# Optimization experiments

Measured on AMD Instinct MI355X. Metric: run time of the kernel, lower is better.

The kernel has to match this reference:

```python
import jax, jax.numpy as jnp
import numpy as np

EMB_DIM = 64
DICT_SIZE = 512
MOMENTUM = 0.99
EPS = 1e-05


def setup_inputs() -> dict:
    key = jax.random.key(0)
    k1, k2 = jax.random.split(key)
    inp = jax.random.normal(k1, (32, EMB_DIM, 64, 64), dtype=jnp.float32)
    embed = jax.random.normal(k2, (DICT_SIZE, EMB_DIM), dtype=jnp.float32)
    cluster_size = jnp.zeros((DICT_SIZE,), dtype=jnp.float32)
    embed_avg = embed.T  # torch: self.embed.T.clone()
    return {"input": inp, "embed": embed, "cluster_size": cluster_size, "embed_avg": embed_avg}


def reference(input, embed, cluster_size, embed_avg):
    b, c, h, w = input.shape
    D = embed.shape[0]
    # torch: input.transpose(1, -1).reshape(-1, emb_dim)  -> row order (b, w, h)
    flatten = jnp.swapaxes(input, 1, -1).reshape(-1, c)  # (N, c)
    # negative squared L2 scores (largest == nearest), as in _torch_knn
    scores = 2.0 * (flatten @ embed.T)                     # (N, D)
    scores = scores - jnp.sum(embed * embed, axis=1)[None, :]
    scores = scores - jnp.sum(flatten * flatten, axis=1)[:, None]
    ids_flat = jnp.argmax(scores, axis=1)                  # (N,) int
    # torch: ids.view(b, h, w) (quirk: flatten order is (b,w,h); h==w so shapes match)
    ids = ids_flat.reshape(b, h, w)
    # lookup: F.embedding(ids, embed).transpose(1, -1); the two transposes cancel
    quantized = jnp.swapaxes(embed[ids_flat].reshape(b, w, h, c), 1, -1)  # (b, c, h, w)
    commit_loss = jnp.mean(jnp.square(input - quantized))
    # EMA codebook statistics (training branch, done under no_grad in torch)
    onehot_sum = jax.ops.segment_sum(jnp.ones_like(ids_flat, dtype=flatten.dtype), ids_flat, num_segments=D)  # (D,)
    embed_sum = jax.ops.segment_sum(flatten, ids_flat, num_segments=D).T  # (c, D) == flatten.T @ onehot
    new_cluster_size = cluster_size * MOMENTUM + onehot_sum * (1.0 - MOMENTUM)
    new_embed_avg = embed_avg * MOMENTUM + embed_sum * (1.0 - MOMENTUM)
    n = jnp.sum(new_cluster_size)
    cs = n * (new_cluster_size + EPS) / (n + D * EPS)
    new_embed = new_embed_avg.T / cs[:, None]
    return quantized, commit_loss, ids, new_embed, new_cluster_size, new_embed_avg
```

## Files before the change

### kernel.cpp

```cpp
#include <hip/hip_runtime.h>

#define EMB 64
#define DICT 512
#define HW 4096
#define NPTS (32 * HW)
#define MOM 0.99f
#define OMOM 0.01f
#define EPSV 1e-5f

typedef float v4f __attribute__((ext_vector_type(4)));
typedef unsigned int uint;
typedef uint uint4v __attribute__((ext_vector_type(4)));
typedef short short8 __attribute__((ext_vector_type(8)));
typedef __bf16 bf16x8 __attribute__((ext_vector_type(8)));
typedef float f32x4 __attribute__((ext_vector_type(4)));

#define WS_COMMIT 0
#define WS_COUNTS 64
#define WS_ESUM   1024
#define WS_ZERO_FLOATS 33792
#define WS_EE     33792
#define WS_EHG    34320
#define WS_IDS    67600

#define PS 520
#define TB 4160

#define ESCALE 65536.0f
#define EINV   (1.0f / 65536.0f)

__device__ __forceinline__ uint bf16rne(float x) {
    uint u = __float_as_uint(x);
    return (u + 0x7fffu + ((u >> 16) & 1u)) >> 16;
}

__device__ __forceinline__ bf16x8 ldfragg(const uint* s, int idx) {
    return __builtin_bit_cast(bf16x8, *(const short8*)(s + idx));
}

__global__ __launch_bounds__(256) void vq_prep(const float* __restrict__ embed,
                                               float* __restrict__ ws,
                                               uint* __restrict__ ehg,
                                               float* __restrict__ ee) {
    int t = threadIdx.x;
    int blk = blockIdx.x;
    for (int i = blk * 256 + t; i < WS_ZERO_FLOATS; i += 32 * 256) ws[i] = 0.f;

    int jl = t >> 4;
    int ci = t & 15;
    int j  = blk * 16 + jl;
    float nrm = 0.f;
    #pragma unroll
    for (int it = 0; it < 2; ++it) {
        int c2 = ci + it * 16;
        float x0 = embed[j * 64 + 2 * c2];
        float x1 = embed[j * 64 + 2 * c2 + 1];
        nrm = fmaf(x0, x0, nrm);
        nrm = fmaf(x1, x1, nrm);
        uint h0 = bf16rne(x0), h1 = bf16rne(x1);
        int plane = (c2 >> 4) * 4 + ((c2 >> 2) & 3);
        int idx = (j >> 7) * TB + plane * PS + (j & 127) * 4 + (c2 & 3);
        ehg[idx] = h0 | (h1 << 16);
    }
    #pragma unroll
    for (int off = 8; off > 0; off >>= 1) nrm += __shfl_xor(nrm, off, 16);
    if (ci == 0) ee[j] = nrm;
}

__global__ __launch_bounds__(256, 4) void vq_argmax(
    const float* __restrict__ input, const uint* __restrict__ ehg,
    const float* __restrict__ ee, const float* __restrict__ embed,
    float* __restrict__ out_q, float* __restrict__ out_ids,
    int* __restrict__ ws_ids, float* __restrict__ ws) {
    __shared__ float sX[16 * PS];
    __shared__ float sEE[512];
    __shared__ int sCand[256];
    __shared__ float sRes[256];
    __shared__ float cred[4];

    int t = threadIdx.x;
    int blk = blockIdx.x;
    int b = blk >> 5, h2 = blk & 31;

    {
        int p = t & 127;
        const float* xg = input + (size_t)b * (EMB * HW) + h2 * 128 + p;
        int ch0 = (t >> 7) * 32;
        #pragma unroll
        for (int i = 0; i < 32; ++i) {
            int ch = ch0 + i;
            sX[(ch >> 2) * PS + p * 4 + (ch & 3)] = xg[(size_t)ch * HW];
        }
        sEE[t] = ee[t];
        sEE[t + 256] = ee[t + 256];
    }
    __syncthreads();

    int l = t & 63, wv = t >> 6;
    int g = l >> 4, col = l & 15;

    bf16x8 Ah[2][2];
    #pragma unroll
    for (int mt = 0; mt < 2; ++mt)
        #pragma unroll
        for (int kh = 0; kh < 2; ++kh) {
            int row = wv * 32 + mt * 16 + col;
            int p0 = kh * 8 + g * 2;
            v4f xa = *(const v4f*)&sX[p0 * PS + row * 4];
            v4f xb = *(const v4f*)&sX[(p0 + 1) * PS + row * 4];
            uint4v fr;
            fr[0] = bf16rne(xa[0]) | (bf16rne(xa[1]) << 16);
            fr[1] = bf16rne(xa[2]) | (bf16rne(xa[3]) << 16);
            fr[2] = bf16rne(xb[0]) | (bf16rne(xb[1]) << 16);
            fr[3] = bf16rne(xb[2]) | (bf16rne(xb[3]) << 16);
            Ah[mt][kh] = __builtin_bit_cast(bf16x8, fr);
        }

    float tb1[2][4], tb2[2][4];
    #pragma unroll
    for (int mt = 0; mt < 2; ++mt)
        #pragma unroll
        for (int r = 0; r < 4; ++r) { tb1[mt][r] = -3.0e38f; tb2[mt][r] = -3.0e38f; }

    for (int jt = 0; jt < 4; ++jt) {
        const uint* eh = ehg + jt * TB;
        #pragma unroll
        for (int nt = 0; nt < 8; ++nt) {
            int i0 = (0 * 4 + g) * PS + (nt * 16 + col) * 4;
            int i1x = (1 * 4 + g) * PS + (nt * 16 + col) * 4;
            bf16x8 Bh0 = ldfragg(eh, i0);
            bf16x8 Bh1 = ldfragg(eh, i1x);
            float e2 = -0.5f * sEE[jt * 128 + nt * 16 + col];
            f32x4 acc0 = {e2, e2, e2, e2};
            f32x4 acc1 = acc0;
            acc0 = __builtin_amdgcn_mfma_f32_16x16x32_bf16(Ah[0][0], Bh0, acc0, 0, 0, 0);
            acc1 = __builtin_amdgcn_mfma_f32_16x16x32_bf16(Ah[1][0], Bh0, acc1, 0, 0, 0);
            acc0 = __builtin_amdgcn_mfma_f32_16x16x32_bf16(Ah[0][1], Bh1, acc0, 0, 0, 0);
            acc1 = __builtin_amdgcn_mfma_f32_16x16x32_bf16(Ah[1][1], Bh1, acc1, 0, 0, 0);
            uint tag = (uint)(511 - (jt * 128 + nt * 16 + col));
            #pragma unroll
            for (int r = 0; r < 4; ++r) {
                float sp0 = __uint_as_float(
                    (__float_as_uint(acc0[r]) & 0xFFFFFE00u) | tag);
                float o1 = tb1[0][r];
                tb1[0][r] = fmaxf(sp0, o1);
                tb2[0][r] = __builtin_amdgcn_fmed3f(sp0, o1, tb2[0][r]);
                float sp1 = __uint_as_float(
                    (__float_as_uint(acc1[r]) & 0xFFFFFE00u) | tag);
                float p1 = tb1[1][r];
                tb1[1][r] = fmaxf(sp1, p1);
                tb2[1][r] = __builtin_amdgcn_fmed3f(sp1, p1, tb2[1][r]);
            }
        }
    }

    #pragma unroll
    for (int mt = 0; mt < 2; ++mt)
        #pragma unroll
        for (int r = 0; r < 4; ++r) {
            float t1 = tb1[mt][r], t2 = tb2[mt][r];
            #pragma unroll
            for (int off = 8; off > 0; off >>= 1) {
                float o1 = __shfl_xor(t1, off, 16);
                float o2 = __shfl_xor(t2, off, 16);
                float hi = fmaxf(t1, o1);
                float lo = fminf(t1, o1);
                t2 = fmaxf(lo, fmaxf(t2, o2));
                t1 = hi;
            }
            if (col == 0) {
                int p = wv * 32 + mt * 16 + g * 4 + r;
                sCand[p * 2]     = 511 - (int)(__float_as_uint(t1) & 511u);
                sCand[p * 2 + 1] = 511 - (int)(__float_as_uint(t2) & 511u);
            }
        }
    __syncthreads();

    int p = t & 127, wc = t >> 7;
    int c = sCand[p * 2 + wc];
    const v4f* erow = (const v4f*)(embed + c * 64);
    float dot = 0.f;
    #pragma unroll
    for (int plane = 0; plane < 16; ++plane) {
        v4f xq = *(const v4f*)&sX[plane * PS + p * 4];
        v4f e4 = erow[plane];
        dot = fmaf(xq[0], e4[0], dot);
        dot = fmaf(xq[1], e4[1], dot);
        dot = fmaf(xq[2], e4[2], dot);
        dot = fmaf(xq[3], e4[3], dot);
    }
    float sx = fmaf(2.f, dot, -sEE[c]);
    sRes[t] = sx;
    __syncthreads();
    float so = sRes[t ^ 128];
    int co = sCand[p * 2 + (1 - wc)];
    bool win = (sx > so) || (sx == so && c < co);

    float cl = 0.f;
    if (win) {
        int h = (h2 << 1) + (p >> 6), w = p & 63;
        ws_ids[b * HW + h2 * 128 + p] = c;
        out_ids[b * HW + w * 64 + h] = (float)c;
        float* qg = out_q + (size_t)b * (EMB * HW) + h2 * 128 + p;
        #pragma unroll
        for (int plane = 0; plane < 16; ++plane) {
            v4f xq = *(const v4f*)&sX[plane * PS + p * 4];
            v4f e4 = erow[plane];
            #pragma unroll
            for (int v = 0; v < 4; ++v) {
                int ch = plane * 4 + v;
                qg[(size_t)ch * HW] = e4[v];
                float d = xq[v] - e4[v];
                cl = fmaf(d, d, cl);
            }
        }
    }
    #pragma unroll
    for (int off = 32; off > 0; off >>= 1) cl += __shfl_down(cl, off);
    if ((t & 63) == 0) cred[t >> 6] = cl;
    __syncthreads();
    if (t == 0)
        unsafeAtomicAdd(&ws[WS_COMMIT], (cred[0] + cred[1]) + (cred[2] + cred[3]));
}

__global__ __launch_bounds__(256) void vq_stats(
    const float* __restrict__ input, const int* __restrict__ ws_ids,
    float* __restrict__ ws) {
    __shared__ uint es[2 * 520];
    __shared__ uint cnt_s[DICT];

    int t = threadIdx.x;
    int bc = blockIdx.x;
    int b = bc >> 5, cg = bc & 31;

    #pragma unroll
    for (int i = t; i < 2 * 520; i += 256) es[i] = 0u;
    if (cg == 0)
        for (int i = t; i < DICT; i += 256) cnt_s[i] = 0u;

    const int* idg = ws_ids + b * HW;
    int4 idv[4];
    #pragma unroll
    for (int it = 0; it < 4; ++it)
        idv[it] = *(const int4*)(idg + (t + it * 256) * 4);
    __syncthreads();

    #pragma unroll
    for (int chl = 0; chl < 2; ++chl) {
        const float* xg = input + (size_t)b * (EMB * HW) + (size_t)(cg * 2 + chl) * HW;
        uint* esr = es + chl * 520;
        #pragma unroll
        for (int it = 0; it < 4; ++it) {
            v4f x = *(const v4f*)(xg + (t + it * 256) * 4);
            atomicAdd(&esr[idv[it].x], (uint)__float2int_rn(x.x * ESCALE));
            atomicAdd(&esr[idv[it].y], (uint)__float2int_rn(x.y * ESCALE));
            atomicAdd(&esr[idv[it].z], (uint)__float2int_rn(x.z * ESCALE));
            atomicAdd(&esr[idv[it].w], (uint)__float2int_rn(x.w * ESCALE));
        }
    }
    if (cg == 0) {
        #pragma unroll
        for (int it = 0; it < 4; ++it) {
            atomicAdd(&cnt_s[idv[it].x], 1u);
            atomicAdd(&cnt_s[idv[it].y], 1u);
            atomicAdd(&cnt_s[idv[it].z], 1u);
            atomicAdd(&cnt_s[idv[it].w], 1u);
        }
    }
    __syncthreads();

    #pragma unroll
    for (int i = t; i < 2 * DICT; i += 256) {
        int chl = i >> 9, j = i & 511;
        int v = (int)es[chl * 520 + j];
        if (v != 0)
            unsafeAtomicAdd(&ws[WS_ESUM + (cg * 2 + chl) * DICT + j],
                            (float)v * EINV);
    }
    if (cg == 0)
        for (int i = t; i < DICT; i += 256) {
            uint c = cnt_s[i];
            if (c != 0u) unsafeAtomicAdd(&ws[WS_COUNTS + i], (float)c);
        }
}

__global__ __launch_bounds__(256) void vq_fin(
    const float* __restrict__ embed_avg, const float* __restrict__ cluster_size,
    const float* __restrict__ ws, float* __restrict__ out_embed,
    float* __restrict__ out_cs, float* __restrict__ out_avg,
    float* __restrict__ out_loss) {
    __shared__ float red[256];
    int t = threadIdx.x, blk = blockIdx.x;

    float ncs0 = cluster_size[t] * MOM + ws[WS_COUNTS + t] * OMOM;
    float ncs1 = cluster_size[t + 256] * MOM + ws[WS_COUNTS + t + 256] * OMOM;
    if (blk == 0) {
        out_cs[t] = ncs0;
        out_cs[t + 256] = ncs1;
        if (t == 0)
            out_loss[0] = ws[WS_COMMIT] * (1.0f / (float)((size_t)NPTS * EMB));
    }
    red[t] = ncs0 + ncs1;
    __syncthreads();
    #pragma unroll
    for (int off = 128; off > 0; off >>= 1) {
        if (t < off) red[t] += red[t + off];
        __syncthreads();
    }
    float n = red[0];

    int idx = blk * 256 + t;
    int ch = idx >> 9, d = idx & 511;
    float avg = embed_avg[idx] * MOM + ws[WS_ESUM + idx] * OMOM;
    out_avg[idx] = avg;
    float ncs = cluster_size[d] * MOM + ws[WS_COUNTS + d] * OMOM;
    float cs = n * (ncs + EPSV) / (n + (float)DICT * EPSV);
    out_embed[d * EMB + ch] = avg / cs;
}

extern "C" void kernel_launch(void* const* d_in, const int* in_sizes, int n_in,
                              void* d_out, int out_size, void* d_ws, size_t ws_size,
                              hipStream_t stream) {
    const float* input        = (const float*)d_in[0];
    const float* embed        = (const float*)d_in[1];
    const float* cluster_size = (const float*)d_in[2];
    const float* embed_avg    = (const float*)d_in[3];

    float* out   = (float*)d_out;
    float* q     = out;
    float* loss  = out + 8388608;
    float* ids   = out + 8388609;
    float* oemb  = out + 8519681;
    float* ocs   = out + 8552449;
    float* oavg  = out + 8552961;
    float* ws    = (float*)d_ws;

    vq_prep  <<<32, 256, 0, stream>>>(embed, ws, (uint*)(ws + WS_EHG), ws + WS_EE);
    vq_argmax<<<1024, 256, 0, stream>>>(input, (const uint*)(ws + WS_EHG),
                                        ws + WS_EE, embed, q, ids,
                                        (int*)(ws + WS_IDS), ws);
    vq_stats <<<1024, 256, 0, stream>>>(input, (const int*)(ws + WS_IDS), ws);
    vq_fin   <<<128, 256, 0, stream>>>(embed_avg, cluster_size, ws, oemb, ocs,
                                       oavg, loss);
}
```

Before: 66.56 us.

## Halve argmax tile to 64 points per block, drop shared input staging

Each argmax block now handles 64 points instead of 128, with one MFMA row tile per wave and twice as many blocks. Input fragments are loaded straight from global memory into registers instead of being staged through a shared-memory tile, and the rescoring and commit-loss passes re-read the input from global. With fewer registers and less LDS per block, the launch bound rises to 8 blocks per SM for higher occupancy. The cost is that each block re-streams the codebook fragments, so total codebook traffic doubles, and the input is read again from global memory (likely served by cache). Only half the threads do the rescoring step.

```diff
diff --git a/kernel.cpp b/kernel.cpp
--- a/kernel.cpp
+++ b/kernel.cpp
@@ -67,151 +67,131 @@
     if (ci == 0) ee[j] = nrm;
 }
 
-__global__ __launch_bounds__(256, 4) void vq_argmax(
+__global__ __launch_bounds__(256, 8) void vq_argmax(
     const float* __restrict__ input, const uint* __restrict__ ehg,
     const float* __restrict__ ee, const float* __restrict__ embed,
     float* __restrict__ out_q, float* __restrict__ out_ids,
     int* __restrict__ ws_ids, float* __restrict__ ws) {
-    __shared__ float sX[16 * PS];
     __shared__ float sEE[512];
-    __shared__ int sCand[256];
-    __shared__ float sRes[256];
+    __shared__ int sCand[128];
+    __shared__ float sRes[128];
     __shared__ float cred[4];
 
     int t = threadIdx.x;
     int blk = blockIdx.x;
-    int b = blk >> 5, h2 = blk & 31;
-
-    {
-        int p = t & 127;
-        const float* xg = input + (size_t)b * (EMB * HW) + h2 * 128 + p;
-        int ch0 = (t >> 7) * 32;
-        #pragma unroll
-        for (int i = 0; i < 32; ++i) {
-            int ch = ch0 + i;
-            sX[(ch >> 2) * PS + p * 4 + (ch & 3)] = xg[(size_t)ch * HW];
-        }
-        sEE[t] = ee[t];
-        sEE[t + 256] = ee[t + 256];
-    }
-    __syncthreads();
+    int b = blk >> 6, region = blk & 63;
+
+    sEE[t] = ee[t];
+    sEE[t + 256] = ee[t + 256];
 
     int l = t & 63, wv = t >> 6;
     int g = l >> 4, col = l & 15;
-
-    bf16x8 Ah[2][2];
-    #pragma unroll
-    for (int mt = 0; mt < 2; ++mt)
-        #pragma unroll
-        for (int kh = 0; kh < 2; ++kh) {
-            int row = wv * 32 + mt * 16 + col;
-            int p0 = kh * 8 + g * 2;
-            v4f xa = *(const v4f*)&sX[p0 * PS + row * 4];
-            v4f xb = *(const v4f*)&sX[(p0 + 1) * PS + row * 4];
-            uint4v fr;
-            fr[0] = bf16rne(xa[0]) | (bf16rne(xa[1]) << 16);
-            fr[1] = bf16rne(xa[2]) | (bf16rne(xa[3]) << 16);
-            fr[2] = bf16rne(xb[0]) | (bf16rne(xb[1]) << 16);
-            fr[3] = bf16rne(xb[2]) | (bf16rne(xb[3]) << 16);
-            Ah[mt][kh] = __builtin_bit_cast(bf16x8, fr);
-        }
-
-    float tb1[2][4], tb2[2][4];
-    #pragma unroll
-    for (int mt = 0; mt < 2; ++mt)
-        #pragma unroll
-        for (int r = 0; r < 4; ++r) { tb1[mt][r] = -3.0e38f; tb2[mt][r] = -3.0e38f; }
+    int row = wv * 16 + col;
+
+    const float* xg = input + (size_t)b * (EMB * HW) + region * 64;
+
+    bf16x8 Ah[2];
+    #pragma unroll
+    for (int kh = 0; kh < 2; ++kh) {
+        int ch0 = kh * 32 + g * 8;
+        uint4v fr;
+        #pragma unroll
+        for (int v = 0; v < 4; ++v) {
+            float x0 = xg[(size_t)(ch0 + 2 * v) * HW + row];
+            float x1 = xg[(size_t)(ch0 + 2 * v + 1) * HW + row];
+            fr[v] = bf16rne(x0) | (bf16rne(x1) << 16);
+        }
+        Ah[kh] = __builtin_bit_cast(bf16x8, fr);
+    }
+    __syncthreads();
+
+    float tb1[4], tb2[4];
+    #pragma unroll
+    for (int r = 0; r < 4; ++r) { tb1[r] = -3.0e38f; tb2[r] = -3.0e38f; }
 
     for (int jt = 0; jt < 4; ++jt) {
         const uint* eh = ehg + jt * TB;
         #pragma unroll
         for (int nt = 0; nt < 8; ++nt) {
-            int i0 = (0 * 4 + g) * PS + (nt * 16 + col) * 4;
-            int i1x = (1 * 4 + g) * PS + (nt * 16 + col) * 4;
-            bf16x8 Bh0 = ldfragg(eh, i0);
-            bf16x8 Bh1 = ldfragg(eh, i1x);
+            bf16x8 Bh0 = ldfragg(eh, (0 * 4 + g) * PS + (nt * 16 + col) * 4);
+            bf16x8 Bh1 = ldfragg(eh, (1 * 4 + g) * PS + (nt * 16 + col) * 4);
             float e2 = -0.5f * sEE[jt * 128 + nt * 16 + col];
-            f32x4 acc0 = {e2, e2, e2, e2};
-            f32x4 acc1 = acc0;
-            acc0 = __builtin_amdgcn_mfma_f32_16x16x32_bf16(Ah[0][0], Bh0, acc0, 0, 0, 0);
-            acc1 = __builtin_amdgcn_mfma_f32_16x16x32_bf16(Ah[1][0], Bh0, acc1, 0, 0, 0);
-            acc0 = __builtin_amdgcn_mfma_f32_16x16x32_bf16(Ah[0][1], Bh1, acc0, 0, 0, 0);
-            acc1 = __builtin_amdgcn_mfma_f32_16x16x32_bf16(Ah[1][1], Bh1, acc1, 0, 0, 0);
+            f32x4 acc = {e2, e2, e2, e2};
+            acc = __builtin_amdgcn_mfma_f32_16x16x32_bf16(Ah[0], Bh0, acc, 0, 0, 0);
+            acc = __builtin_amdgcn_mfma_f32_16x16x32_bf16(Ah[1], Bh1, acc, 0, 0, 0);
             uint tag = (uint)(511 - (jt * 128 + nt * 16 + col));
             #pragma unroll
             for (int r = 0; r < 4; ++r) {
-                float sp0 = __uint_as_float(
-                    (__float_as_uint(acc0[r]) & 0xFFFFFE00u) | tag);
-                float o1 = tb1[0][r];
-                tb1[0][r] = fmaxf(sp0, o1);
-                tb2[0][r] = __builtin_amdgcn_fmed3f(sp0, o1, tb2[0][r]);
-                float sp1 = __uint_as_float(
-                    (__float_as_uint(acc1[r]) & 0xFFFFFE00u) | tag);
-                float p1 = tb1[1][r];
-                tb1[1][r] = fmaxf(sp1, p1);
-                tb2[1][r] = __builtin_amdgcn_fmed3f(sp1, p1, tb2[1][r]);
+                float sp = __uint_as_float(
+                    (__float_as_uint(acc[r]) & 0xFFFFFE00u) | tag);
+                float o1 = tb1[r];
+                tb1[r] = fmaxf(sp, o1);
+                tb2[r] = __builtin_amdgcn_fmed3f(sp, o1, tb2[r]);
             }
         }
     }
 
     #pragma unroll
-    for (int mt = 0; mt < 2; ++mt)
-        #pragma unroll
-        for (int r = 0; r < 4; ++r) {
-            float t1 = tb1[mt][r], t2 = tb2[mt][r];
-            #pragma unroll
-            for (int off = 8; off > 0; off >>= 1) {
-                float o1 = __shfl_xor(t1, off, 16);
-                float o2 = __shfl_xor(t2, off, 16);
-                float hi = fmaxf(t1, o1);
-                float lo = fminf(t1, o1);
-                t2 = fmaxf(lo, fmaxf(t2, o2));
-                t1 = hi;
-            }
-            if (col == 0) {
-                int p = wv * 32 + mt * 16 + g * 4 + r;
-                sCand[p * 2]     = 511 - (int)(__float_as_uint(t1) & 511u);
-                sCand[p * 2 + 1] = 511 - (int)(__float_as_uint(t2) & 511u);
-            }
-        }
-    __syncthreads();
-
-    int p = t & 127, wc = t >> 7;
-    int c = sCand[p * 2 + wc];
-    const v4f* erow = (const v4f*)(embed + c * 64);
-    float dot = 0.f;
-    #pragma unroll
-    for (int plane = 0; plane < 16; ++plane) {
-        v4f xq = *(const v4f*)&sX[plane * PS + p * 4];
-        v4f e4 = erow[plane];
-        dot = fmaf(xq[0], e4[0], dot);
-        dot = fmaf(xq[1], e4[1], dot);
-        dot = fmaf(xq[2], e4[2], dot);
-        dot = fmaf(xq[3], e4[3], dot);
-    }
-    float sx = fmaf(2.f, dot, -sEE[c]);
-    sRes[t] = sx;
-    __syncthreads();
-    float so = sRes[t ^ 128];
-    int co = sCand[p * 2 + (1 - wc)];
-    bool win = (sx > so) || (sx == so && c < co);
-
-    float cl = 0.f;
-    if (win) {
-        int h = (h2 << 1) + (p >> 6), w = p & 63;
-        ws_ids[b * HW + h2 * 128 + p] = c;
-        out_ids[b * HW + w * 64 + h] = (float)c;
-        float* qg = out_q + (size_t)b * (EMB * HW) + h2 * 128 + p;
+    for (int r = 0; r < 4; ++r) {
+        float t1 = tb1[r], t2 = tb2[r];
+        #pragma unroll
+        for (int off = 8; off > 0; off >>= 1) {
+            float o1 = __shfl_xor(t1, off, 16);
+            float o2 = __shfl_xor(t2, off, 16);
+            float hi = fmaxf(t1, o1);
+            float lo = fminf(t1, o1);
+            t2 = fmaxf(lo, fmaxf(t2, o2));
+            t1 = hi;
+        }
+        if (col == 0) {
+            int p = wv * 16 + g * 4 + r;
+            sCand[p * 2]     = 511 - (int)(__float_as_uint(t1) & 511u);
+            sCand[p * 2 + 1] = 511 - (int)(__float_as_uint(t2) & 511u);
+        }
+    }
+    __syncthreads();
+
+    int p = t & 63, wc = (t >> 6) & 1;
+    int c = 0;
+    if (t < 128) {
+        c = sCand[p * 2 + wc];
+        const v4f* erow = (const v4f*)(embed + c * 64);
+        float dot = 0.f;
         #pragma unroll
         for (int plane = 0; plane < 16; ++plane) {
-            v4f xq = *(const v4f*)&sX[plane * PS + p * 4];
             v4f e4 = erow[plane];
             #pragma unroll
             for (int v = 0; v < 4; ++v) {
-                int ch = plane * 4 + v;
-                qg[(size_t)ch * HW] = e4[v];
-                float d = xq[v] - e4[v];
-                cl = fmaf(d, d, cl);
+                float x = xg[(size_t)(plane * 4 + v) * HW + p];
+                dot = fmaf(x, e4[v], dot);
+            }
+        }
+        sRes[t] = fmaf(2.f, dot, -sEE[c]);
+    }
+    __syncthreads();
+
+    float cl = 0.f;
+    if (t < 128) {
+        float sx = sRes[t];
+        float so = sRes[t ^ 64];
+        int co = sCand[p * 2 + (1 - wc)];
+        bool win = (sx > so) || (sx == so && c < co);
+        if (win) {
+            ws_ids[b * HW + region * 64 + p] = c;
+            out_ids[b * HW + p * 64 + region] = (float)c;
+            float* qg = out_q + (size_t)b * (EMB * HW) + region * 64 + p;
+            const v4f* erow = (const v4f*)(embed + c * 64);
+            #pragma unroll
+            for (int plane = 0; plane < 16; ++plane) {
+                v4f e4 = erow[plane];
+                #pragma unroll
+                for (int v = 0; v < 4; ++v) {
+                    int ch = plane * 4 + v;
+                    float x = xg[(size_t)ch * HW + p];
+                    qg[(size_t)ch * HW] = e4[v];
+                    float d = x - e4[v];
+                    cl = fmaf(d, d, cl);
+                }
             }
         }
     }
@@ -336,7 +316,7 @@
     float* ws    = (float*)d_ws;
 
     vq_prep  <<<32, 256, 0, stream>>>(embed, ws, (uint*)(ws + WS_EHG), ws + WS_EE);
-    vq_argmax<<<1024, 256, 0, stream>>>(input, (const uint*)(ws + WS_EHG),
+    vq_argmax<<<2048, 256, 0, stream>>>(input, (const uint*)(ws + WS_EHG),
                                         ws + WS_EE, embed, q, ids,
                                         (int*)(ws + WS_IDS), ws);
     vq_stats <<<1024, 256, 0, stream>>>(input, (const int*)(ws + WS_IDS), ws);
```

New measurement: 79.69 us. +19.7%, slower.
